# Kernel optimization log

Hardware: AMD Instinct MI355X
Metric: run time of the kernel (lower is better)

## Reference

```python
import jax, jax.numpy as jnp
import numpy as np

NUM_HEADS = 32
NUM_KV_HEADS = 8
HEAD_DIM = 128
N_REP = NUM_HEADS // NUM_KV_HEADS
BLOCK = 256  # kvcache_block_size
NUM_BLOCKS = 32
BATCH = 4
SEQ = 1024
N_TOK = BATCH * SEQ

# scale is computed in the torch module as (1/sqrt(head_dim)) rounded to bfloat16
SCALE = jnp.float32(jnp.asarray(1.0 / np.sqrt(HEAD_DIM), dtype=jnp.bfloat16))


def setup_inputs() -> dict:
    key = jax.random.key(0)
    kq, kk, kv = jax.random.split(key, 3)
    q = jax.random.normal(kq, (N_TOK, NUM_HEADS, HEAD_DIM), dtype=jnp.float32)
    k = jax.random.normal(kk, (N_TOK, NUM_KV_HEADS, HEAD_DIM), dtype=jnp.float32)
    v = jax.random.normal(kv, (N_TOK, NUM_KV_HEADS, HEAD_DIM), dtype=jnp.float32)
    k_cache = jnp.zeros((NUM_BLOCKS, BLOCK, NUM_KV_HEADS, HEAD_DIM), dtype=jnp.float32)
    v_cache = jnp.zeros_like(k_cache)
    slot_mapping = jnp.arange(N_TOK, dtype=jnp.int64 if jax.config.jax_enable_x64 else jnp.int32)
    cu = jnp.arange(BATCH + 1, dtype=jnp.int32) * SEQ
    return {"q": q, "k": k, "v": v, "k_cache": k_cache, "v_cache": v_cache,
            "slot_mapping": slot_mapping, "cu_seqlens_q": cu, "cu_seqlens_k": cu}


def _store_kvcache(k, v, k_cache, v_cache, slot_mapping):
    # scatter store of new K/V into paged cache; invalid slots are dropped
    blk = slot_mapping // BLOCK
    inner = slot_mapping % BLOCK
    valid = (slot_mapping != -1) & (blk < k_cache.shape[0]) & (inner < BLOCK)
    blk = jnp.where(valid, blk, k_cache.shape[0])  # out-of-range -> dropped
    k_cache = k_cache.at[blk, inner].set(k, mode="drop")
    v_cache = v_cache.at[blk, inner].set(v, mode="drop")
    return k_cache, v_cache


def _prefill_attn(q, k, v):
    # packed varlen batch with uniform seq lengths -> dense [B,S,...] causal GQA attention
    qb = q.reshape(BATCH, SEQ, NUM_HEADS, HEAD_DIM)
    kb = jnp.repeat(k.reshape(BATCH, SEQ, NUM_KV_HEADS, HEAD_DIM), N_REP, axis=2)  # repeat_kv
    vb = jnp.repeat(v.reshape(BATCH, SEQ, NUM_KV_HEADS, HEAD_DIM), N_REP, axis=2)
    scores = jnp.einsum("bqhd,bkhd->bhqk", qb, kb) * SCALE  # [B,H,S,S]
    causal = jnp.tril(jnp.ones((SEQ, SEQ), dtype=bool))
    scores = jnp.where(causal, scores, -jnp.inf)
    # torch code clamps to [-100, 100] before softmax (masked -inf becomes -100)
    probs = jax.nn.softmax(jnp.clip(scores, -100.0, 100.0), axis=-1)
    out = jnp.einsum("bhqk,bkhd->bqhd", probs, vb)
    return out.reshape(N_TOK, NUM_HEADS * HEAD_DIM)


def reference(q, k, v, k_cache, v_cache, slot_mapping, cu_seqlens_q, cu_seqlens_k):
    k_cache, v_cache = _store_kvcache(k, v, k_cache, v_cache, slot_mapping)
    o = _prefill_attn(q, k, v)
    return o, k_cache, v_cache
```

## Files before the change

kernel.cpp:

```cpp
#include <hip/hip_runtime.h>
#include <math.h>
#include <string.h>

#define BB 4
#define SS 1024
#define HH 32
#define GG 8
#define DD 128
#define NTOK (BB*SS)
#define NBLK 32
#define BLKSZ 256
#define CACHE_ELEMS ((size_t)NBLK*BLKSZ*GG*DD)

typedef __attribute__((ext_vector_type(8)))  short  short8;
typedef __attribute__((ext_vector_type(16))) float  floatx16;

union FragU { unsigned u[4]; uint4 u4; short8 s8; };

__device__ __forceinline__ unsigned pack_bf16x2(float a, float b) {
    unsigned ua = __builtin_bit_cast(unsigned, a);
    unsigned ub = __builtin_bit_cast(unsigned, b);
    ua = (ua + 0x7FFFu + ((ua >> 16) & 1u)) >> 16;
    ub = (ub + 0x7FFFu + ((ub >> 16) & 1u)) & 0xFFFF0000u;
    return ua | ub;
}

#if __has_builtin(__builtin_amdgcn_permlane32_swap)
#define HAVE_PL32 1
#endif

__device__ __forceinline__ unsigned cvt_pk_bf16(float lo, float hi) {
    unsigned r;
    asm("v_cvt_pk_bf16_f32 %0, %1, %2" : "=v"(r) : "v"(lo), "v"(hi));
    return r;
}

__device__ __forceinline__ float xhalf_max(float x) {
#ifdef HAVE_PL32
    unsigned u = __builtin_bit_cast(unsigned, x);
    auto r = __builtin_amdgcn_permlane32_swap(u, u, false, false);
    return fmaxf(__builtin_bit_cast(float, (unsigned)r[0]),
                 __builtin_bit_cast(float, (unsigned)r[1]));
#else
    return fmaxf(x, __shfl_xor(x, 32));
#endif
}
__device__ __forceinline__ float xhalf_add(float x) {
#ifdef HAVE_PL32
    unsigned u = __builtin_bit_cast(unsigned, x);
    auto r = __builtin_amdgcn_permlane32_swap(u, u, false, false);
    return __builtin_bit_cast(float, (unsigned)r[0]) +
           __builtin_bit_cast(float, (unsigned)r[1]);
#else
    return x + __shfl_xor(x, 32);
#endif
}

__device__ __forceinline__ FragU make_pfrag(const unsigned* pk, int s2, int hb) {
    FragU pf;
#ifdef HAVE_PL32
    auto ra = __builtin_amdgcn_permlane32_swap(pk[4 * s2],     pk[4 * s2 + 2], false, false);
    auto rb = __builtin_amdgcn_permlane32_swap(pk[4 * s2 + 1], pk[4 * s2 + 3], false, false);
    pf.u[0] = (unsigned)ra[0]; pf.u[1] = (unsigned)rb[0];
    pf.u[2] = (unsigned)ra[1]; pf.u[3] = (unsigned)rb[1];
#else
    unsigned px0 = (unsigned)__shfl_xor((int)pk[4 * s2],     32);
    unsigned px1 = (unsigned)__shfl_xor((int)pk[4 * s2 + 1], 32);
    unsigned px2 = (unsigned)__shfl_xor((int)pk[4 * s2 + 2], 32);
    unsigned px3 = (unsigned)__shfl_xor((int)pk[4 * s2 + 3], 32);
    if (hb == 0) { pf.u[0] = pk[4*s2];   pf.u[1] = pk[4*s2+1]; pf.u[2] = px0; pf.u[3] = px1; }
    else         { pf.u[0] = px2; pf.u[1] = px3; pf.u[2] = pk[4*s2+2]; pf.u[3] = pk[4*s2+3]; }
#endif
    return pf;
}

__global__ void prep_kv(const float* __restrict__ k, const float* __restrict__ v,
                        const int* __restrict__ slot_mapping,
                        uint4* __restrict__ ksw, uint4* __restrict__ vsw,
                        float* __restrict__ kco, float* __restrict__ vco) {
    __shared__ float lds[32 * 132];
    const int t = threadIdx.x;
    const int kt = blockIdx.x, gy = blockIdx.y, b = blockIdx.z;
    const int isv = gy >> 3, g = gy & 7;
    const float* sp = (isv ? v : k) + ((size_t)(b * SS + kt * 32) * GG + g) * DD;
    float* dco = isv ? vco : kco;
    #pragma unroll
    for (int i = 0; i < 4; ++i) {
        int u = t + 256 * i;
        int row = u >> 5, c4 = u & 31;
        float4 f = *(const float4*)(sp + (size_t)row * (GG * DD) + c4 * 4);
        float* lp = &lds[row * 132 + c4 * 4];
        lp[0] = f.x; lp[1] = f.y; lp[2] = f.z; lp[3] = f.w;
        int slot = slot_mapping[b * SS + kt * 32 + row];
        if ((unsigned)slot < (unsigned)(NBLK * BLKSZ))
            *(float4*)(dco + (size_t)slot * (GG * DD) + g * DD + c4 * 4) = f;
    }
    __syncthreads();
    const int lane = t & 63, hb = lane >> 5, l31 = lane & 31;
    const size_t tbase = ((size_t)(b * GG + g) * 32 + kt) * 8;
    if (!isv) {
        #pragma unroll
        for (int i = 0; i < 2; ++i) {
            int s = (t >> 6) + 4 * i;
            const float* lp = &lds[l31 * 132 + s * 16 + hb * 8];
            uint4 o;
            o.x = pack_bf16x2(lp[0], lp[1]); o.y = pack_bf16x2(lp[2], lp[3]);
            o.z = pack_bf16x2(lp[4], lp[5]); o.w = pack_bf16x2(lp[6], lp[7]);
            ksw[(tbase + s) * 64 + lane] = o;
        }
    } else {
        #pragma unroll
        for (int i = 0; i < 2; ++i) {
            int f8 = (t >> 6) + 4 * i;
            int t4 = f8 >> 1, s2 = f8 & 1;
            int keyb = s2 * 16 + hb * 8;
            int d = t4 * 32 + l31;
            uint4 o;
            o.x = pack_bf16x2(lds[(keyb + 0) * 132 + d], lds[(keyb + 1) * 132 + d]);
            o.y = pack_bf16x2(lds[(keyb + 2) * 132 + d], lds[(keyb + 3) * 132 + d]);
            o.z = pack_bf16x2(lds[(keyb + 4) * 132 + d], lds[(keyb + 5) * 132 + d]);
            o.w = pack_bf16x2(lds[(keyb + 6) * 132 + d], lds[(keyb + 7) * 132 + d]);
            vsw[(tbase + f8) * 64 + lane] = o;
        }
    }
}

__global__ void copy_cache2(const float4* __restrict__ s0, const float4* __restrict__ s1,
                            float4* __restrict__ d0, float4* __restrict__ d1) {
    const size_t half = CACHE_ELEMS / 4;
    size_t i = (size_t)blockIdx.x * 256 + threadIdx.x;
    if (i < half) d0[i] = s0[i];
    else          d1[i - half] = s1[i - half];
}

__global__ __launch_bounds__(256, 2)
void attn_kernel(const float* __restrict__ q,
                 const uint4* __restrict__ ksw,
                 const uint4* __restrict__ vsw,
                 float* __restrict__ out, float sc2 ) {
    const int lane = threadIdx.x & 63;
    const int wave = threadIdx.x >> 6;
    const int l31  = lane & 31;
    const int hb   = lane >> 5;

    const int wg  = blockIdx.x;
    const int xcd = wg & 7;
    const int sl  = wg >> 3;
    const int bg  = xcd * 4 + (sl >> 4);
    const int pr  = sl & 15;
    const int b   = bg >> 3, g = bg & 7;
    const int h   = g * 4 + wave;
    const int tb  = b * SS;

    const uint4* kln = ksw + (size_t)bg * (32 * 8 * 64) + lane;
    const uint4* vln = vsw + (size_t)bg * (32 * 8 * 64) + lane;

    #pragma unroll 1
    for (int half = 0; half < 2; ++half) {
        const int qt = half ? pr : (31 - pr);
        const int q0 = qt * 32;

        short8 qf[8];
        const float* qp = q + ((size_t)(tb + q0 + l31) * HH + h) * DD;
        #pragma unroll
        for (int s = 0; s < 8; ++s) {
            int d0 = s * 16 + hb * 8;
            float4 f0 = *(const float4*)(qp + d0);
            float4 f1 = *(const float4*)(qp + d0 + 4);
            FragU fr;
            fr.u[0] = pack_bf16x2(f0.x, f0.y); fr.u[1] = pack_bf16x2(f0.z, f0.w);
            fr.u[2] = pack_bf16x2(f1.x, f1.y); fr.u[3] = pack_bf16x2(f1.z, f1.w);
            qf[s] = fr.s8;
        }

        floatx16 oacc[4] = {};
        float m = -__builtin_inff(), l = 0.f;

        uint4 kA[8], kB[8], vv[8];
        #pragma unroll
        for (int s = 0; s < 8; ++s) kA[s] = kln[s * 64];

        auto body = [&](uint4 (&kc)[8], uint4 (&kn)[8], int kt) {
            if (kt < qt) {
                #pragma unroll
                for (int s = 0; s < 8; ++s) kn[s] = kln[(kt + 1) * 512 + s * 64];
            }
            #pragma unroll
            for (int s = 0; s < 8; ++s) vv[s] = vln[kt * 512 + s * 64];

            floatx16 st = {};
            __builtin_amdgcn_s_setprio(1);
            #pragma unroll
            for (int s = 0; s < 8; ++s) {
                FragU ka; ka.u4 = kc[s];
                st = __builtin_amdgcn_mfma_f32_32x32x16_bf16(ka.s8, qf[s], st, 0, 0, 0);
            }
            __builtin_amdgcn_s_setprio(0);

            float e[16];
            #pragma unroll
            for (int r = 0; r < 16; ++r) {
                float v = st[r];
                if (kt == qt) {
                    int row = (r & 3) + 8 * (r >> 2) + 4 * hb;
                    if (row > l31) v = -__builtin_inff();
                }
                e[r] = v;
            }
            float trm[8];
            #pragma unroll
            for (int i = 0; i < 8; ++i) trm[i] = fmaxf(e[i], e[i + 8]);
            #pragma unroll
            for (int i = 0; i < 4; ++i) trm[i] = fmaxf(trm[i], trm[i + 4]);
            float tmax = fmaxf(fmaxf(trm[0], trm[2]), fmaxf(trm[1], trm[3]));
            tmax = xhalf_max(tmax) * sc2;

            if (__any(tmax > m + 8.f)) {
                const float mnew  = fmaxf(m, tmax);
                const float alpha = exp2f(m - mnew);
                #pragma unroll
                for (int tt = 0; tt < 4; ++tt)
                    #pragma unroll
                    for (int r = 0; r < 16; ++r) oacc[tt][r] *= alpha;
                l *= alpha;
                m = mnew;
            }

            #pragma unroll
            for (int r = 0; r < 16; ++r) e[r] = exp2f(fmaf(e[r], sc2, -m));
            float sr[8];
            #pragma unroll
            for (int i = 0; i < 8; ++i) sr[i] = e[i] + e[i + 8];
            #pragma unroll
            for (int i = 0; i < 4; ++i) sr[i] += sr[i + 4];
            float psum = (sr[0] + sr[1]) + (sr[2] + sr[3]);
            l += xhalf_add(psum);

            unsigned pk[8];
            #pragma unroll
            for (int u2 = 0; u2 < 8; ++u2) pk[u2] = cvt_pk_bf16(e[2 * u2], e[2 * u2 + 1]);

            __builtin_amdgcn_s_setprio(1);
            #pragma unroll
            for (int s2 = 0; s2 < 2; ++s2) {
                FragU pf = make_pfrag(pk, s2, hb);
                #pragma unroll
                for (int t4 = 0; t4 < 4; ++t4) {
                    FragU vf; vf.u4 = vv[t4 * 2 + s2];
                    oacc[t4] = __builtin_amdgcn_mfma_f32_32x32x16_bf16(vf.s8, pf.s8, oacc[t4], 0, 0, 0);
                }
            }
            __builtin_amdgcn_s_setprio(0);
        };

        int kt = 0;
        #pragma unroll 1
        for (;;) {
            body(kA, kB, kt);
            if (++kt > qt) break;
            body(kB, kA, kt);
            if (++kt > qt) break;
        }

        const float inv_l = 1.f / l;
        float* op = out + ((size_t)(tb + q0 + l31) * HH + h) * DD;
        #pragma unroll
        for (int t4 = 0; t4 < 4; ++t4) {
            #pragma unroll
            for (int grp = 0; grp < 4; ++grp) {
                float4 o4;
                o4.x = oacc[t4][grp * 4 + 0] * inv_l; o4.y = oacc[t4][grp * 4 + 1] * inv_l;
                o4.z = oacc[t4][grp * 4 + 2] * inv_l; o4.w = oacc[t4][grp * 4 + 3] * inv_l;
                *(float4*)(op + t4 * 32 + grp * 8 + hb * 4) = o4;
            }
        }
    }
}

extern "C" void kernel_launch(void* const* d_in, const int* in_sizes, int n_in,
                              void* d_out, int out_size, void* d_ws, size_t ws_size,
                              hipStream_t stream) {
    const float* q     = (const float*)d_in[0];
    const float* k     = (const float*)d_in[1];
    const float* v     = (const float*)d_in[2];
    const float* kc_in = (const float*)d_in[3];
    const float* vc_in = (const float*)d_in[4];
    const int*   slot  = (const int*)d_in[5];

    float* o_out  = (float*)d_out;
    float* kc_out = o_out + (size_t)NTOK * HH * DD;
    float* vc_out = kc_out + CACHE_ELEMS;

    uint4* ksw = (uint4*)d_ws;
    uint4* vsw = ksw + (size_t)BB * GG * 32 * 8 * 64;

    float sc = 1.0f / sqrtf((float)DD);
    unsigned u; memcpy(&u, &sc, 4);
    u = (u + 0x7FFFu + ((u >> 16) & 1u)) & 0xFFFF0000u;
    memcpy(&sc, &u, 4);
    const float sc2 = sc * 1.44269504088896340736f;

    copy_cache2<<<(int)(CACHE_ELEMS / 4 / 256) * 2, 256, 0, stream>>>(
        (const float4*)kc_in, (const float4*)vc_in, (float4*)kc_out, (float4*)vc_out);
    prep_kv<<<dim3(32, GG * 2, BB), 256, 0, stream>>>(k, v, slot, ksw, vsw, kc_out, vc_out);
    attn_kernel<<<512, 256, 0, stream>>>(q, ksw, vsw, o_out, sc2);
}
```

Baseline: 314.3 us.

## Software-pipeline QK^T MFMA one tile ahead of softmax and PV

Restructures the attention inner loop so the QK^T MFMAs for the next key tile are issued before the softmax and PV work of the current tile, with K loads prefetched two tiles ahead and V loads one tile ahead. The goal is to overlap matrix-core work with the VALU-heavy softmax and to hide global load latency. The cost is a second score accumulator plus another K buffer in registers, which raises VGPR pressure and may lower occupancy.

```diff
diff --git a/kernel.cpp b/kernel.cpp
--- a/kernel.cpp
+++ b/kernel.cpp
@@ -177,26 +177,21 @@
         float m = -__builtin_inff(), l = 0.f;
 
         uint4 kA[8], kB[8], vv[8];
-        #pragma unroll
-        for (int s = 0; s < 8; ++s) kA[s] = kln[s * 64];
-
-        auto body = [&](uint4 (&kc)[8], uint4 (&kn)[8], int kt) {
-            if (kt < qt) {
-                #pragma unroll
-                for (int s = 0; s < 8; ++s) kn[s] = kln[(kt + 1) * 512 + s * 64];
-            }
-            #pragma unroll
-            for (int s = 0; s < 8; ++s) vv[s] = vln[kt * 512 + s * 64];
-
+        floatx16 stA = {}, stB = {};
+
+        auto qk8 = [&](const uint4 (&kk)[8]) -> floatx16 {
             floatx16 st = {};
             __builtin_amdgcn_s_setprio(1);
             #pragma unroll
             for (int s = 0; s < 8; ++s) {
-                FragU ka; ka.u4 = kc[s];
+                FragU ka; ka.u4 = kk[s];
                 st = __builtin_amdgcn_mfma_f32_32x32x16_bf16(ka.s8, qf[s], st, 0, 0, 0);
             }
             __builtin_amdgcn_s_setprio(0);
-
+            return st;
+        };
+
+        auto finish = [&](const floatx16& st, int kt) {
             float e[16];
             #pragma unroll
             for (int r = 0; r < 16; ++r) {
@@ -253,12 +248,36 @@
             __builtin_amdgcn_s_setprio(0);
         };
 
+        auto body = [&](const floatx16& st_cur, floatx16& st_nxt,
+                        uint4 (&kload)[8], const uint4 (&kqk)[8], int kt) {
+            if (kt + 1 <= qt) st_nxt = qk8(kqk);
+            if (kt + 2 <= qt) {
+                #pragma unroll
+                for (int s = 0; s < 8; ++s) kload[s] = kln[(kt + 2) * 512 + s * 64];
+            }
+            finish(st_cur, kt);
+            if (kt + 1 <= qt) {
+                #pragma unroll
+                for (int s = 0; s < 8; ++s) vv[s] = vln[(kt + 1) * 512 + s * 64];
+            }
+        };
+
+        #pragma unroll
+        for (int s = 0; s < 8; ++s) kA[s] = kln[s * 64];
+        if (qt >= 1) {
+            #pragma unroll
+            for (int s = 0; s < 8; ++s) kB[s] = kln[512 + s * 64];
+        }
+        stA = qk8(kA);
+        #pragma unroll
+        for (int s = 0; s < 8; ++s) vv[s] = vln[s * 64];
+
         int kt = 0;
         #pragma unroll 1
         for (;;) {
-            body(kA, kB, kt);
+            body(stA, stB, kA, kB, kt);
             if (++kt > qt) break;
-            body(kB, kA, kt);
+            body(stB, stA, kB, kA, kt);
             if (++kt > qt) break;
         }
 
```

New measurement: 340.4 us. +8.3%, slower.
